# Optimization experiments

Measured on AMD Instinct MI355X. Metric: run time of the kernel, lower is better.

The kernel has to match this reference:

```python
import jax, jax.numpy as jnp
import numpy as np

# CPC config (mirrors CONFIG in the torch repo)
B, S, D = 16, 128, 256      # batch, seq_len, latent dim
K = 12                      # CONFIG.num_predicts
N = 128                     # CONFIG.negative_samples
W = S - K                   # prediction window


def setup_inputs() -> dict:
    key = jax.random.key(0)
    k1, k2, k3, k4 = jax.random.split(key, 4)
    return {
        "predictions": jax.random.normal(k1, (B, W, K, D), jnp.float32),
        "latent": jax.random.normal(k2, (B, S, D), jnp.float32),
        # negative-sample indices (torch generated these with a torch.Generator)
        "batch_idx": jax.random.randint(k3, (N * W * B,), 0, B, jnp.int32),
        "seq_idx": jax.random.randint(k4, (N * W * B,), 1, S, jnp.int32),
    }


def reference(predictions, latent, batch_idx, seq_idx):
    B_, S_, D_ = latent.shape
    _, W_, K_, _ = predictions.shape
    N_ = batch_idx.shape[0] // (W_ * B_)

    # --- sample_for_prediction: gather negatives -------------------------
    # base_idx: arange(W) broadcast to (B, N, W), flattened (matches torch)
    base = jnp.broadcast_to(jnp.arange(W_, dtype=jnp.int32), (B_, N_, W_)).reshape(-1)
    seq = jnp.remainder(seq_idx + base, S_)
    ext = seq + batch_idx * S_
    neg = latent.reshape(-1, D_)[ext].reshape(B_, N_, W_, D_)  # [B,N,W,D]

    # positives: for step k (1..K), pos_k = latent[:, k : k+W]
    pos_idx = jnp.arange(1, K_ + 1)[:, None] + jnp.arange(W_)[None, :]  # [K,W]
    pos = latent[:, pos_idx]  # [B,K,W,D]

    # --- scores: (pred * sample).mean(dim=-1) as contractions -----------
    inv_d = 1.0 / D_
    pos_s = jnp.einsum('bwkd,bkwd->bkw', predictions, pos) * inv_d        # [B,K,W]
    neg_s = jnp.einsum('bwkd,bnwd->bknw', predictions, neg) * inv_d       # [B,K,N,W]
    logits = jnp.concatenate([pos_s[:, :, None, :], neg_s], axis=2)       # [B,K,1+N,W]

    # --- cross-entropy with target class 0, mean over B*W ---------------
    losses = jnp.mean(jax.nn.logsumexp(logits, axis=2) - logits[:, :, 0, :], axis=(0, 2))  # [K]
    acc = jnp.mean((jnp.argmax(logits, axis=2) == 0).astype(jnp.float32), axis=(0, 2))     # [K]
    return losses, acc
```

## Files before the change

kernel.cpp:

```cpp
#include <hip/hip_runtime.h>
#include <hip/hip_bf16.h>

#define BB 16
#define SS 128
#define DD 256
#define KK 12
#define NN 128
#define WW 116

typedef __attribute__((ext_vector_type(8))) short short8;
typedef __attribute__((ext_vector_type(4))) float f32x4;

__device__ __forceinline__ int swz(int byte_off, int row) {
    return byte_off ^ ((row & 7) << 4);
}

__device__ __forceinline__ void cvt_hilo8(const float4 p, const float4 q,
                                          short8& h, short8& l) {
    float x[8] = {p.x, p.y, p.z, p.w, q.x, q.y, q.z, q.w};
#pragma unroll
    for (int i = 0; i < 8; ++i) {
        __hip_bfloat16 hb = __float2bfloat16(x[i]);
        float hf = __bfloat162float(hb);
        __hip_bfloat16 lb = __float2bfloat16(x[i] - hf);
        h[i] = __builtin_bit_cast(short, hb);
        l[i] = __builtin_bit_cast(short, lb);
    }
}

__global__ __launch_bounds__(256, 4)
void cpc_main(const float* __restrict__ pred,
              const float* __restrict__ latent,
              const int* __restrict__ bidx,
              const int* __restrict__ sidx,
              float* __restrict__ out) {
    const int wg = blockIdx.x;
    const int b  = wg / WW;
    const int w  = wg - b * WW;
    const int t  = threadIdx.x;

    __shared__ short Ahi[16 * DD];
    __shared__ short Alo[16 * DD];
    __shared__ float sc[KK][NN + 1];
    __shared__ float posv[KK];

    const float* __restrict__ pbase = pred + (size_t)wg * KK * DD;

    if (t < 96) {
        const int r = t >> 3, seg = t & 7;
        const float* src = pbase + r * DD + seg * 32;
#pragma unroll
        for (int c = 0; c < 4; ++c) {
            float4 p = *reinterpret_cast<const float4*>(src + c * 8);
            float4 q = *reinterpret_cast<const float4*>(src + c * 8 + 4);
            short8 h, l;
            cvt_hilo8(p, q, h, l);
            const int byte = r * 512 + seg * 64 + c * 16;
            *reinterpret_cast<short8*>((char*)Ahi + swz(byte, r)) = h;
            *reinterpret_cast<short8*>((char*)Alo + swz(byte, r)) = l;
        }
    } else if (t < 128) {
        const int u = t - 96;
        const int r = 12 + (u >> 3), seg = u & 7;
        const short8 z = {0, 0, 0, 0, 0, 0, 0, 0};
#pragma unroll
        for (int c = 0; c < 4; ++c) {
            const int byte = r * 512 + seg * 64 + c * 16;
            *reinterpret_cast<short8*>((char*)Ahi + swz(byte, r)) = z;
            *reinterpret_cast<short8*>((char*)Alo + swz(byte, r)) = z;
        }
    }

    const int wv   = t >> 6;
    const int lane = t & 63;
    const int lr   = lane & 15;
    const int lg   = lane >> 4;
    const int n0 = wv * 32 + lr;
    const int n1 = n0 + 16;
    const int i0 = (b * NN + n0) * WW + w;
    const int i1 = (b * NN + n1) * WW + w;
    const int ext0 = ((sidx[i0] + w) & (SS - 1)) + bidx[i0] * SS;
    const int ext1 = ((sidx[i1] + w) & (SS - 1)) + bidx[i1] * SS;
    const float* __restrict__ L0 = latent + (size_t)ext0 * DD + lg * 8;
    const float* __restrict__ L1 = latent + (size_t)ext1 * DD + lg * 8;

    __syncthreads();

    f32x4 acc0 = {0.f, 0.f, 0.f, 0.f};
    f32x4 acc1 = {0.f, 0.f, 0.f, 0.f};
    const int abyte = lr * 512 + lg * 16;
#pragma unroll 2
    for (int ks = 0; ks < 8; ++ks) {
        const short8 ah = *reinterpret_cast<const short8*>(
            (const char*)Ahi + swz(abyte + ks * 64, lr));
        const short8 al = *reinterpret_cast<const short8*>(
            (const char*)Alo + swz(abyte + ks * 64, lr));
        const float4 p0 = *reinterpret_cast<const float4*>(L0 + ks * 32);
        const float4 q0 = *reinterpret_cast<const float4*>(L0 + ks * 32 + 4);
        const float4 p1 = *reinterpret_cast<const float4*>(L1 + ks * 32);
        const float4 q1 = *reinterpret_cast<const float4*>(L1 + ks * 32 + 4);
        short8 bh0, bl0, bh1, bl1;
        cvt_hilo8(p0, q0, bh0, bl0);
        cvt_hilo8(p1, q1, bh1, bl1);
        acc0 = __builtin_amdgcn_mfma_f32_16x16x32_bf16(ah, bh0, acc0, 0, 0, 0);
        acc1 = __builtin_amdgcn_mfma_f32_16x16x32_bf16(ah, bh1, acc1, 0, 0, 0);
        acc0 = __builtin_amdgcn_mfma_f32_16x16x32_bf16(ah, bl0, acc0, 0, 0, 0);
        acc1 = __builtin_amdgcn_mfma_f32_16x16x32_bf16(ah, bl1, acc1, 0, 0, 0);
        acc0 = __builtin_amdgcn_mfma_f32_16x16x32_bf16(al, bh0, acc0, 0, 0, 0);
        acc1 = __builtin_amdgcn_mfma_f32_16x16x32_bf16(al, bh1, acc1, 0, 0, 0);
    }

    constexpr float inv_d = 1.0f / DD;
    const int krow = lg * 4;
    if (krow < KK) {
#pragma unroll
        for (int r = 0; r < 4; ++r) {
            sc[krow + r][n0] = acc0[r] * inv_d;
            sc[krow + r][n1] = acc1[r] * inv_d;
        }
    }

    if (t < 96) {
        const int k = t >> 3, g = t & 7;
        const float* pr = pbase + k * DD + g * 32;
        const float* lrow = latent + ((size_t)b * SS + (w + k + 1)) * DD + g * 32;
        float s = 0.f;
#pragma unroll
        for (int d = 0; d < 32; d += 4) {
            const float4 pv = *reinterpret_cast<const float4*>(pr + d);
            const float4 lv = *reinterpret_cast<const float4*>(lrow + d);
            s = fmaf(pv.x, lv.x, s); s = fmaf(pv.y, lv.y, s);
            s = fmaf(pv.z, lv.z, s); s = fmaf(pv.w, lv.w, s);
        }
        s += __shfl_xor(s, 1);
        s += __shfl_xor(s, 2);
        s += __shfl_xor(s, 4);
        if (g == 0) posv[k] = s * inv_d;
    }
    __syncthreads();

    if (t < 96) {
        const int k = t >> 3, g = t & 7;
        const float p = posv[k];
        float v[16];
        float m = p;
#pragma unroll
        for (int j = 0; j < 16; ++j) {
            v[j] = sc[k][j * 8 + g];
            m = fmaxf(m, v[j]);
        }
        m = fmaxf(m, __shfl_xor(m, 1));
        m = fmaxf(m, __shfl_xor(m, 2));
        m = fmaxf(m, __shfl_xor(m, 4));
        float sum = (g == 0) ? __expf(p - m) : 0.f;
#pragma unroll
        for (int j = 0; j < 16; ++j) sum += __expf(v[j] - m);
        sum += __shfl_xor(sum, 1);
        sum += __shfl_xor(sum, 2);
        sum += __shfl_xor(sum, 4);
        if (g == 0) {
            constexpr float inv_bw = 1.0f / (BB * WW);
            const float lse = m + __logf(sum);
            atomicAdd(&out[k], (lse - p) * inv_bw);
            atomicAdd(&out[KK + k], (p >= m) ? inv_bw : 0.f);
        }
    }
}

extern "C" void kernel_launch(void* const* d_in, const int* in_sizes, int n_in,
                              void* d_out, int out_size, void* d_ws, size_t ws_size,
                              hipStream_t stream) {
    const float* pred   = (const float*)d_in[0];
    const float* latent = (const float*)d_in[1];
    const int*   bidx   = (const int*)d_in[2];
    const int*   sidx   = (const int*)d_in[3];
    float* out = (float*)d_out;
    hipMemsetAsync(out, 0, 2 * KK * sizeof(float), stream);
    cpc_main<<<BB * WW, 256, 0, stream>>>(pred, latent, bidx, sidx, out);
}
```

Measured before the change: 160.7 us.

## Precompute bf16 hi/lo splits in a pre-pass and prefetch gathered rows

Adds a separate kernel that converts all of predictions and latent once into bf16 high and low halves in workspace. The main kernel then loads ready-made bf16 operands instead of redoing the split for every gathered negative row. The K-loop is fully unrolled with register double-buffering of the next gathered chunk. This removes repeated per-element VALU conversion work, but adds an extra launch and a full write-and-reread of the large predictions tensor, which did not need converting since each block reads its slice only once.

```diff
diff --git a/kernel.cpp b/kernel.cpp
--- a/kernel.cpp
+++ b/kernel.cpp
@@ -8,6 +8,9 @@
 #define NN 128
 #define WW 116
 
+#define NPRED (BB * WW * KK * DD)
+#define NLAT  (BB * SS * DD)
+
 typedef __attribute__((ext_vector_type(8))) short short8;
 typedef __attribute__((ext_vector_type(4))) float f32x4;
 
@@ -15,21 +18,38 @@
     return byte_off ^ ((row & 7) << 4);
 }
 
-__device__ __forceinline__ void cvt_hilo8(const float4 p, const float4 q,
-                                          short8& h, short8& l) {
-    float x[8] = {p.x, p.y, p.z, p.w, q.x, q.y, q.z, q.w};
-#pragma unroll
-    for (int i = 0; i < 8; ++i) {
+__global__ __launch_bounds__(256)
+void cvt_split(const float* __restrict__ pred, const float* __restrict__ latent,
+               ushort* __restrict__ Phi, ushort* __restrict__ Plo,
+               ushort* __restrict__ Lhi, ushort* __restrict__ Llo) {
+    const int g  = blockIdx.x * 256 + threadIdx.x;
+    const int i4 = g * 4;
+    const float* src; ushort* dh; ushort* dl; int off;
+    if (i4 < NPRED)      { src = pred;   dh = Phi; dl = Plo; off = i4; }
+    else                 { off = i4 - NPRED;
+                           if (off >= NLAT) return;
+                           src = latent; dh = Lhi; dl = Llo; }
+    const float4 v = *reinterpret_cast<const float4*>(src + off);
+    float x[4] = {v.x, v.y, v.z, v.w};
+    ushort h[4], l[4];
+#pragma unroll
+    for (int i = 0; i < 4; ++i) {
         __hip_bfloat16 hb = __float2bfloat16(x[i]);
         float hf = __bfloat162float(hb);
         __hip_bfloat16 lb = __float2bfloat16(x[i] - hf);
-        h[i] = __builtin_bit_cast(short, hb);
-        l[i] = __builtin_bit_cast(short, lb);
-    }
+        h[i] = __builtin_bit_cast(ushort, hb);
+        l[i] = __builtin_bit_cast(ushort, lb);
+    }
+    ushort4 hv; hv.x = h[0]; hv.y = h[1]; hv.z = h[2]; hv.w = h[3];
+    ushort4 lv; lv.x = l[0]; lv.y = l[1]; lv.z = l[2]; lv.w = l[3];
+    *reinterpret_cast<ushort4*>(dh + off) = hv;
+    *reinterpret_cast<ushort4*>(dl + off) = lv;
 }
 
 __global__ __launch_bounds__(256, 4)
-void cpc_main(const float* __restrict__ pred,
+void cpc_main(const ushort* __restrict__ Phi, const ushort* __restrict__ Plo,
+              const ushort* __restrict__ Lhi, const ushort* __restrict__ Llo,
+              const float* __restrict__ pred,
               const float* __restrict__ latent,
               const int* __restrict__ bidx,
               const int* __restrict__ sidx,
@@ -39,22 +59,19 @@
     const int w  = wg - b * WW;
     const int t  = threadIdx.x;
 
-    __shared__ short Ahi[16 * DD];
-    __shared__ short Alo[16 * DD];
+    __shared__ ushort Ahi[16 * DD];
+    __shared__ ushort Alo[16 * DD];
     __shared__ float sc[KK][NN + 1];
     __shared__ float posv[KK];
 
-    const float* __restrict__ pbase = pred + (size_t)wg * KK * DD;
-
     if (t < 96) {
         const int r = t >> 3, seg = t & 7;
-        const float* src = pbase + r * DD + seg * 32;
+        const ushort* sh = Phi + ((size_t)wg * KK + r) * DD + seg * 32;
+        const ushort* sl = Plo + ((size_t)wg * KK + r) * DD + seg * 32;
 #pragma unroll
         for (int c = 0; c < 4; ++c) {
-            float4 p = *reinterpret_cast<const float4*>(src + c * 8);
-            float4 q = *reinterpret_cast<const float4*>(src + c * 8 + 4);
-            short8 h, l;
-            cvt_hilo8(p, q, h, l);
+            const short8 h = *reinterpret_cast<const short8*>(sh + c * 8);
+            const short8 l = *reinterpret_cast<const short8*>(sl + c * 8);
             const int byte = r * 512 + seg * 64 + c * 16;
             *reinterpret_cast<short8*>((char*)Ahi + swz(byte, r)) = h;
             *reinterpret_cast<short8*>((char*)Alo + swz(byte, r)) = l;
@@ -81,33 +98,40 @@
     const int i1 = (b * NN + n1) * WW + w;
     const int ext0 = ((sidx[i0] + w) & (SS - 1)) + bidx[i0] * SS;
     const int ext1 = ((sidx[i1] + w) & (SS - 1)) + bidx[i1] * SS;
-    const float* __restrict__ L0 = latent + (size_t)ext0 * DD + lg * 8;
-    const float* __restrict__ L1 = latent + (size_t)ext1 * DD + lg * 8;
+    const ushort* __restrict__ L0h = Lhi + (size_t)ext0 * DD + lg * 8;
+    const ushort* __restrict__ L0l = Llo + (size_t)ext0 * DD + lg * 8;
+    const ushort* __restrict__ L1h = Lhi + (size_t)ext1 * DD + lg * 8;
+    const ushort* __restrict__ L1l = Llo + (size_t)ext1 * DD + lg * 8;
 
     __syncthreads();
 
     f32x4 acc0 = {0.f, 0.f, 0.f, 0.f};
     f32x4 acc1 = {0.f, 0.f, 0.f, 0.f};
+    short8 ch0 = *reinterpret_cast<const short8*>(L0h);
+    short8 cl0 = *reinterpret_cast<const short8*>(L0l);
+    short8 ch1 = *reinterpret_cast<const short8*>(L1h);
+    short8 cl1 = *reinterpret_cast<const short8*>(L1l);
     const int abyte = lr * 512 + lg * 16;
-#pragma unroll 2
+#pragma unroll
     for (int ks = 0; ks < 8; ++ks) {
+        short8 nh0, nl0, nh1, nl1;
+        if (ks < 7) {
+            nh0 = *reinterpret_cast<const short8*>(L0h + (ks + 1) * 32);
+            nl0 = *reinterpret_cast<const short8*>(L0l + (ks + 1) * 32);
+            nh1 = *reinterpret_cast<const short8*>(L1h + (ks + 1) * 32);
+            nl1 = *reinterpret_cast<const short8*>(L1l + (ks + 1) * 32);
+        }
         const short8 ah = *reinterpret_cast<const short8*>(
             (const char*)Ahi + swz(abyte + ks * 64, lr));
         const short8 al = *reinterpret_cast<const short8*>(
             (const char*)Alo + swz(abyte + ks * 64, lr));
-        const float4 p0 = *reinterpret_cast<const float4*>(L0 + ks * 32);
-        const float4 q0 = *reinterpret_cast<const float4*>(L0 + ks * 32 + 4);
-        const float4 p1 = *reinterpret_cast<const float4*>(L1 + ks * 32);
-        const float4 q1 = *reinterpret_cast<const float4*>(L1 + ks * 32 + 4);
-        short8 bh0, bl0, bh1, bl1;
-        cvt_hilo8(p0, q0, bh0, bl0);
-        cvt_hilo8(p1, q1, bh1, bl1);
-        acc0 = __builtin_amdgcn_mfma_f32_16x16x32_bf16(ah, bh0, acc0, 0, 0, 0);
-        acc1 = __builtin_amdgcn_mfma_f32_16x16x32_bf16(ah, bh1, acc1, 0, 0, 0);
-        acc0 = __builtin_amdgcn_mfma_f32_16x16x32_bf16(ah, bl0, acc0, 0, 0, 0);
-        acc1 = __builtin_amdgcn_mfma_f32_16x16x32_bf16(ah, bl1, acc1, 0, 0, 0);
-        acc0 = __builtin_amdgcn_mfma_f32_16x16x32_bf16(al, bh0, acc0, 0, 0, 0);
-        acc1 = __builtin_amdgcn_mfma_f32_16x16x32_bf16(al, bh1, acc1, 0, 0, 0);
+        acc0 = __builtin_amdgcn_mfma_f32_16x16x32_bf16(ah, ch0, acc0, 0, 0, 0);
+        acc1 = __builtin_amdgcn_mfma_f32_16x16x32_bf16(ah, ch1, acc1, 0, 0, 0);
+        acc0 = __builtin_amdgcn_mfma_f32_16x16x32_bf16(ah, cl0, acc0, 0, 0, 0);
+        acc1 = __builtin_amdgcn_mfma_f32_16x16x32_bf16(ah, cl1, acc1, 0, 0, 0);
+        acc0 = __builtin_amdgcn_mfma_f32_16x16x32_bf16(al, ch0, acc0, 0, 0, 0);
+        acc1 = __builtin_amdgcn_mfma_f32_16x16x32_bf16(al, ch1, acc1, 0, 0, 0);
+        ch0 = nh0; cl0 = nl0; ch1 = nh1; cl1 = nl1;
     }
 
     constexpr float inv_d = 1.0f / DD;
@@ -122,7 +146,7 @@
 
     if (t < 96) {
         const int k = t >> 3, g = t & 7;
-        const float* pr = pbase + k * DD + g * 32;
+        const float* pr = pred + ((size_t)wg * KK + k) * DD + g * 32;
         const float* lrow = latent + ((size_t)b * SS + (w + k + 1)) * DD + g * 32;
         float s = 0.f;
 #pragma unroll
@@ -175,6 +199,15 @@
     const int*   bidx   = (const int*)d_in[2];
     const int*   sidx   = (const int*)d_in[3];
     float* out = (float*)d_out;
+
+    ushort* Phi = (ushort*)d_ws;
+    ushort* Plo = Phi + NPRED;
+    ushort* Lhi = Plo + NPRED;
+    ushort* Llo = Lhi + NLAT;
+
     hipMemsetAsync(out, 0, 2 * KK * sizeof(float), stream);
-    cpc_main<<<BB * WW, 256, 0, stream>>>(pred, latent, bidx, sidx, out);
-}
+    const int ncvt = (NPRED + NLAT) / 4;
+    cvt_split<<<(ncvt + 255) / 256, 256, 0, stream>>>(pred, latent, Phi, Plo, Lhi, Llo);
+    cpc_main<<<BB * WW, 256, 0, stream>>>(Phi, Plo, Lhi, Llo,
+                                          pred, latent, bidx, sidx, out);
+}
```

Measured after the change: 165.9 us. 3.2% more time.
